# Kernel optimization log

Measured on AMD Instinct MI355X. Metric: run time of the kernel, lower is better.

Reference implementation:

```python
import jax, jax.numpy as jnp
import numpy as np

N_NODES = 50000
N_EDGES = 800000
D_IN = 128
D_HID = 128
D_OUT = 128
N_LAYERS = 2
NEG_SLOPE = 0.2


def leaky(x):
    return jnp.where(x >= 0, x, NEG_SLOPE * x)


def setup_inputs() -> dict:
    key = jax.random.key(0)
    ks = jax.random.split(key, 12)
    s = 1.0 / np.sqrt(D_HID)
    feats = jax.random.normal(ks[0], (N_NODES, D_IN), dtype=jnp.float32)
    src = jax.random.randint(ks[1], (N_EDGES,), 0, N_NODES)
    dst = jax.random.randint(ks[2], (N_EDGES,), 0, N_NODES)
    # SIRConv params per layer: W_Q (dst), W_K (src), W_R (output proj)
    Wq = jax.random.normal(ks[3], (N_LAYERS, D_IN, D_HID), dtype=jnp.float32) * s
    bq = jnp.zeros((N_LAYERS, D_HID), dtype=jnp.float32)
    Wk = jax.random.normal(ks[4], (N_LAYERS, D_IN, D_HID), dtype=jnp.float32) * s
    bk = jnp.zeros((N_LAYERS, D_HID), dtype=jnp.float32)
    Wr = jax.random.normal(ks[5], (N_LAYERS, D_HID, D_HID), dtype=jnp.float32) * s
    br = jnp.zeros((N_LAYERS, D_HID), dtype=jnp.float32)
    # Jumping-knowledge readouts: one per entry of feats_list (input + each layer);
    # input_dim == hidden_dim so weights stack along the leading axis.
    Wro = jax.random.normal(ks[6], (N_LAYERS + 1, D_HID, D_OUT), dtype=jnp.float32) * s
    bro = jnp.zeros((N_LAYERS + 1, D_OUT), dtype=jnp.float32)
    return {"feats": feats, "Wq": Wq, "bq": bq, "Wk": Wk, "bk": bk,
            "Wr": Wr, "br": br, "Wro": Wro, "bro": bro,
            "src": src, "dst": dst}


def reference(feats, Wq, bq, Wk, bk, Wr, br, Wro, bro, src, dst):
    # mean-aggregation denominator: in-degree, clamped to 1
    deg = jax.ops.segment_sum(jnp.ones((N_EDGES,), jnp.float32), dst,
                              num_segments=N_NODES)
    denom = jnp.maximum(deg, 1.0)[:, None]  # [N, 1]

    feats_list = [feats]
    h = feats
    for i in range(N_LAYERS):
        hq = h @ Wq[i] + bq[i]          # [N, H] (dst transform)
        hk = h @ Wk[i] + bk[i]          # [N, H] (src transform)
        m = leaky(hq[dst] + hk[src])    # [E, H] contextualized messages
        agg = jax.ops.segment_sum(m, dst, num_segments=N_NODES) / denom
        h = agg @ Wr[i] + br[i]         # conv output (+ residual = 0)
        h = leaky(h)                    # norm='none', dropout=0
        feats_list.append(h)

    # jumping-knowledge readout: sum of per-stage linear readouts
    score = feats_list[0] @ Wro[0] + bro[0]
    for i in range(1, N_LAYERS + 1):
        score = score + feats_list[i] @ Wro[i] + bro[i]
    return score
```

## Files before the change

### kernel.cpp

```cpp
#include <hip/hip_runtime.h>

#define NN 50000
#define NE 800000
#define D 128
#define NEG 0.2f

#define NEB 256
#define TILE1 3125
#define NB2 196
#define CAPB 128
#define NT64 782

#define SB_PREP 576
#define SB_CONV 6250
#define SB_TOTAL (SB_PREP + SB_CONV + NEB)

typedef short bf8_t __attribute__((ext_vector_type(8)));
typedef float f4_t __attribute__((ext_vector_type(4)));

__device__ __forceinline__ unsigned short f2bf(float f) {
  unsigned int u = __float_as_uint(f);
  return (unsigned short)((u + 0x7FFF + ((u >> 16) & 1)) >> 16);
}
__device__ __forceinline__ float bf2f(unsigned int b) { return __uint_as_float(b << 16); }

__device__ __forceinline__ f4_t MF(bf8_t a, bf8_t b, f4_t c) {
  return __builtin_amdgcn_mfma_f32_16x16x32_bf16(a, b, c, 0, 0, 0);
}

__device__ __forceinline__ int swz_u(int u) { return u ^ ((u >> 4) & 7); }

__device__ __forceinline__ int excl_scan256(int x, int t, int* wsum) {
  const int lane = t & 63, wave = t >> 6;
  int v = x;
#pragma unroll
  for (int off = 1; off < 64; off <<= 1) {
    int y = __shfl_up(v, off, 64);
    if (lane >= off) v += y;
  }
  if (lane == 63) wsum[wave] = v;
  __syncthreads();
  int wbase = 0;
  for (int w = 0; w < wave; ++w) wbase += wsum[w];
  return wbase + v - x;
}


__device__ __forceinline__ void stage_wh(unsigned short* wbuf,
                                         const unsigned short* __restrict__ WTh, int t) {
#pragma unroll
  for (int i = 0; i < 4; ++i) {
    int u = t + i * 256;
    *(uint4*)(wbuf + swz_u(u) * 8) = *(const uint4*)(WTh + u * 8);
  }
}

__device__ __forceinline__ void load_a16(const unsigned short* __restrict__ A,
                                         int base, int l15, int quad, bf8_t (&afr)[4]) {
  int r = base + l15;
  if (r >= NN) r = NN - 1;
  const unsigned short* p = A + (size_t)r * D + quad * 8;
#pragma unroll
  for (int kc = 0; kc < 4; ++kc) afr[kc] = *(const bf8_t*)(p + kc * 32);
}

__device__ __forceinline__ void load_a16_lds(const unsigned short* buf, int wave,
                                             int l15, int quad, bf8_t (&afr)[4]) {
  const int r = wave * 16 + l15;
#pragma unroll
  for (int kc = 0; kc < 4; ++kc)
    afr[kc] = *(const bf8_t*)(buf + swz_u(r * 16 + kc * 4 + quad) * 8);
}

__device__ __forceinline__ void tile16h(const unsigned short* wbuf, const bf8_t (&afr)[4],
                                        int l15, int quad, f4_t* acc4) {
#pragma unroll
  for (int kc = 0; kc < 4; ++kc)
#pragma unroll
    for (int nt = 0; nt < 4; ++nt) {
      bf8_t b = *(const bf8_t*)(wbuf + swz_u((nt * 16 + l15) * 16 + kc * 4 + quad) * 8);
      acc4[nt] = MF(afr[kc], b, acc4[nt]);
    }
}

__device__ __forceinline__ void store_c8(unsigned short* __restrict__ C,
                                         const float* __restrict__ bias,
                                         const f4_t (&acc)[8], int base, int l15,
                                         int quad, bool lk) {
#pragma unroll
  for (int j = 0; j < 8; ++j) {
    int col = (j >> 2) * 64 + (j & 3) * 16 + l15;
    float bb = bias[col];
#pragma unroll
    for (int reg = 0; reg < 4; ++reg) {
      int row = base + quad * 4 + reg;
      if (row < NN) {
        float v = acc[j][reg] + bb;
        if (lk) v = v >= 0.f ? v : NEG * v;
        C[(size_t)row * D + col] = f2bf(v);
      }
    }
  }
}

#define ACC_TO_ABUF(ACC, BIAS)                                        \
  {                                                                   \
    _Pragma("unroll") for (int j = 0; j < 8; ++j) {                   \
      int col = (j >> 2) * 64 + (j & 3) * 16 + l15;                   \
      float bb = (BIAS)[col];                                         \
      _Pragma("unroll") for (int reg = 0; reg < 4; ++reg) {           \
        int rl = wave * 16 + quad * 4 + reg;                          \
        float v = ACC[j][reg] + bb;                                   \
        v = v >= 0.f ? v : NEG * v;                                   \
        int s = rl * D + col;                                         \
        abuf[s ^ ((rl & 7) << 3)] = f2bf(v);                          \
      }                                                               \
    }                                                                 \
  }

__global__ __launch_bounds__(256) void setup(
    const float* __restrict__ Wq, const float* __restrict__ Wk,
    const float* __restrict__ Wr, const float* __restrict__ Wro,
    const float* __restrict__ feats, const int* __restrict__ src,
    const int* __restrict__ dst,
    unsigned short* __restrict__ WT, unsigned short* __restrict__ x0,
    unsigned int* __restrict__ ebuf2, int* __restrict__ H_T) {
  __shared__ int cnt[NB2];
  const int b = blockIdx.x;
  const int t = threadIdx.x;
  if (b < SB_PREP) {
    const int m = b >> 6, xb = b & 63;
    const float* sp;
    if (m < 2) sp = Wq + m * D * D;
    else if (m < 4) sp = Wk + (m - 2) * D * D;
    else if (m < 6) sp = Wr + (m - 4) * D * D;
    else sp = Wro + (m - 6) * D * D;
    const int n = xb * 2 + (t >> 7);
    const int k = t & 127;
    WT[(size_t)m * D * D + n * D + k] = f2bf(sp[k * D + n]);
  } else if (b < SB_PREP + SB_CONV) {
    int i = ((b - SB_PREP) * 256 + t) * 4;
    float4 v = *(const float4*)(feats + i);
    ushort4 o = {f2bf(v.x), f2bf(v.y), f2bf(v.z), f2bf(v.w)};
    *(ushort4*)(x0 + i) = o;
  } else {
    const int blk = b - SB_PREP - SB_CONV;
    if (t < NB2) cnt[t] = 0;
    __syncthreads();
    const int beg = blk * TILE1, end = beg + TILE1;
    for (int i = beg + t; i < end; i += 256) {
      unsigned int d = (unsigned int)dst[i];
      unsigned int s = (unsigned int)src[i];
      int bkt = (int)(d >> 8);
      int pos = atomicAdd(&cnt[bkt], 1);
      if (pos < CAPB)
        ebuf2[((size_t)bkt * NEB + blk) * CAPB + pos] = s | (d << 16);
    }
    __syncthreads();
    if (t < NB2) H_T[blk * NB2 + t] = cnt[t];
  }
}

__global__ __launch_bounds__(256) void sort_qk0(
    const int* __restrict__ H_T, const unsigned int* __restrict__ ebuf2,
    int* __restrict__ ssrc, int* __restrict__ rowptr, int* __restrict__ deg,
    const unsigned short* __restrict__ x0,
    const unsigned short* __restrict__ WTq, const float* __restrict__ bq_,
    const unsigned short* __restrict__ WTk, const float* __restrict__ bk_,
    unsigned short* __restrict__ hq, unsigned short* __restrict__ hk) {
  __shared__ __align__(16) unsigned char smraw[16384];
  const int t = threadIdx.x;
  const int gx = blockIdx.x;
  if (gx < NB2) {
    int* cnt = (int*)smraw;
    int* fill = cnt + 256;
    int* sc = fill + 256;
    int* wsum = sc + 256;
    const int b = gx;
    int tot = 0;
    if (t < NB2)
#pragma unroll 4
      for (int j = 0; j < NEB; ++j) tot += H_T[j * NB2 + t];
    int bbase = excl_scan256(tot, t, wsum);
    sc[t] = bbase;
    __syncthreads();
    const int beg = sc[b];
    int cj = H_T[t * NB2 + b];
    if (cj > CAPB) cj = CAPB;
    const unsigned int* cell = ebuf2 + ((size_t)b * NEB + t) * CAPB;
    cnt[t] = 0;
    __syncthreads();
    for (int i = 0; i < cj; ++i)
      atomicAdd(&cnt[(cell[i] >> 16) & 255], 1);
    __syncthreads();
    const int x = cnt[t];
    const int excl = excl_scan256(x, t, wsum);
    fill[t] = excl;
    const int node = (b << 8) + t;
    if (node < NN) {
      rowptr[node] = beg + excl;
      deg[node] = x;
    }
    if (b == 0 && t == 0) rowptr[NN] = NE;
    __syncthreads();
    for (int i = 0; i < cj; ++i) {
      unsigned int p = cell[i];
      int pos = atomicAdd(&fill[(p >> 16) & 255], 1);
      ssrc[beg + pos] = (int)(p & 0xFFFFu);
    }
  } else {
    unsigned short* wbuf = (unsigned short*)smraw;
    const int tile = gx - NB2;
    const int wave = t >> 6, lane = t & 63;
    const int l15 = lane & 15, quad = lane >> 4;
    const int base = tile * 64 + wave * 16;
    bf8_t afr[4];
    load_a16(x0, base, l15, quad, afr);
    stage_wh(wbuf, WTq, t);
    __syncthreads();
    f4_t aq[8] = {};
    tile16h(wbuf, afr, l15, quad, aq);
    __syncthreads();
    stage_wh(wbuf, WTq + 64 * D, t);
    __syncthreads();
    tile16h(wbuf, afr, l15, quad, aq + 4);
    store_c8(hq, bq_, aq, base, l15, quad, false);
    __syncthreads();
    stage_wh(wbuf, WTk, t);
    __syncthreads();
    f4_t ak[8] = {};
    tile16h(wbuf, afr, l15, quad, ak);
    __syncthreads();
    stage_wh(wbuf, WTk + 64 * D, t);
    __syncthreads();
    tile16h(wbuf, afr, l15, quad, ak + 4);
    store_c8(hk, bk_, ak, base, l15, quad, false);
  }
}

#define PROC(kb)                                                     \
  {                                                                  \
    float m;                                                         \
    m = q[0] + bf2f(kb.x & 0xFFFFu); a[0] += m >= 0.f ? m : NEG * m; \
    m = q[1] + bf2f(kb.x >> 16);     a[1] += m >= 0.f ? m : NEG * m; \
    m = q[2] + bf2f(kb.y & 0xFFFFu); a[2] += m >= 0.f ? m : NEG * m; \
    m = q[3] + bf2f(kb.y >> 16);     a[3] += m >= 0.f ? m : NEG * m; \
    m = q[4] + bf2f(kb.z & 0xFFFFu); a[4] += m >= 0.f ? m : NEG * m; \
    m = q[5] + bf2f(kb.z >> 16);     a[5] += m >= 0.f ? m : NEG * m; \
    m = q[6] + bf2f(kb.w & 0xFFFFu); a[6] += m >= 0.f ? m : NEG * m; \
    m = q[7] + bf2f(kb.w >> 16);     a[7] += m >= 0.f ? m : NEG * m; \
  }

__global__ __launch_bounds__(256) void aggregate(
    const int* __restrict__ rowptr, const int* __restrict__ ssrc,
    const int* __restrict__ deg,
    const unsigned short* __restrict__ hq, const unsigned short* __restrict__ hk,
    unsigned short* __restrict__ ag) {
  const int wave = threadIdx.x >> 6, lane = threadIdx.x & 63;
  const int v = blockIdx.x * 4 + wave;
  if (v >= NN) return;
  const int sub = lane & 15, grp = lane >> 4;
  const int beg = rowptr[v], end = rowptr[v + 1];

  uint4 qb = *(const uint4*)(hq + (size_t)v * D + sub * 8);
  float q[8];
  q[0] = bf2f(qb.x & 0xFFFFu); q[1] = bf2f(qb.x >> 16);
  q[2] = bf2f(qb.y & 0xFFFFu); q[3] = bf2f(qb.y >> 16);
  q[4] = bf2f(qb.z & 0xFFFFu); q[5] = bf2f(qb.z >> 16);
  q[6] = bf2f(qb.w & 0xFFFFu); q[7] = bf2f(qb.w >> 16);

  float a[8] = {0.f, 0.f, 0.f, 0.f, 0.f, 0.f, 0.f, 0.f};
  int e = beg + grp;
  for (; e + 12 < end; e += 16) {
    int s0 = ssrc[e];
    int s1 = ssrc[e + 4];
    int s2 = ssrc[e + 8];
    int s3 = ssrc[e + 12];
    uint4 k0 = *(const uint4*)(hk + (size_t)s0 * D + sub * 8);
    uint4 k1 = *(const uint4*)(hk + (size_t)s1 * D + sub * 8);
    uint4 k2 = *(const uint4*)(hk + (size_t)s2 * D + sub * 8);
    uint4 k3 = *(const uint4*)(hk + (size_t)s3 * D + sub * 8);
    PROC(k0);
    PROC(k1);
    PROC(k2);
    PROC(k3);
  }
  for (; e + 4 < end; e += 8) {
    int s0 = ssrc[e];
    int s1 = ssrc[e + 4];
    uint4 k0 = *(const uint4*)(hk + (size_t)s0 * D + sub * 8);
    uint4 k1 = *(const uint4*)(hk + (size_t)s1 * D + sub * 8);
    PROC(k0);
    PROC(k1);
  }
  if (e < end) {
    int s0 = ssrc[e];
    uint4 k0 = *(const uint4*)(hk + (size_t)s0 * D + sub * 8);
    PROC(k0);
  }
#pragma unroll
  for (int j = 0; j < 8; ++j) {
    a[j] += __shfl_xor(a[j], 16, 64);
    a[j] += __shfl_xor(a[j], 32, 64);
  }
  if (grp == 0) {
    float inv = 1.f / fmaxf((float)deg[v], 1.f);
    uint4 o;
    o.x = (unsigned int)f2bf(a[0] * inv) | ((unsigned int)f2bf(a[1] * inv) << 16);
    o.y = (unsigned int)f2bf(a[2] * inv) | ((unsigned int)f2bf(a[3] * inv) << 16);
    o.z = (unsigned int)f2bf(a[4] * inv) | ((unsigned int)f2bf(a[5] * inv) << 16);
    o.w = (unsigned int)f2bf(a[6] * inv) | ((unsigned int)f2bf(a[7] * inv) << 16);
    *(uint4*)(ag + (size_t)v * D + sub * 8) = o;
  }
}

__global__ __launch_bounds__(256) void wr_qk1(
    const unsigned short* __restrict__ ag,
    const unsigned short* __restrict__ WTr, const float* __restrict__ brr,
    unsigned short* __restrict__ h1,
    const unsigned short* __restrict__ WTq, const float* __restrict__ bq1,
    unsigned short* __restrict__ hq,
    const unsigned short* __restrict__ WTk, const float* __restrict__ bk1,
    unsigned short* __restrict__ hk) {
  __shared__ unsigned short wbuf[64 * D];
  __shared__ unsigned short abuf[64 * D];
  const int t = threadIdx.x, wave = t >> 6, lane = t & 63;
  const int l15 = lane & 15, quad = lane >> 4;
  const int tb = blockIdx.x * 64;
  const int base = tb + wave * 16;

  bf8_t afr[4];
  load_a16(ag, base, l15, quad, afr);
  stage_wh(wbuf, WTr, t);
  __syncthreads();
  f4_t acc[8] = {};
  tile16h(wbuf, afr, l15, quad, acc);
  __syncthreads();
  stage_wh(wbuf, WTr + 64 * D, t);
  __syncthreads();
  tile16h(wbuf, afr, l15, quad, acc + 4);

  ACC_TO_ABUF(acc, brr);
  __syncthreads();

  bf8_t hfr[4];
  load_a16_lds(abuf, wave, l15, quad, hfr);
#pragma unroll
  for (int i = 0; i < 4; ++i) {
    int u = t + i * 256;
    int row = tb + (u >> 4);
    if (row < NN)
      *(uint4*)(h1 + (size_t)tb * D + u * 8) = *(const uint4*)(abuf + swz_u(u) * 8);
  }

  stage_wh(wbuf, WTq, t);
  __syncthreads();
  f4_t aq[8] = {};
  tile16h(wbuf, hfr, l15, quad, aq);
  __syncthreads();
  stage_wh(wbuf, WTq + 64 * D, t);
  __syncthreads();
  tile16h(wbuf, hfr, l15, quad, aq + 4);
  store_c8(hq, bq1, aq, base, l15, quad, false);
  __syncthreads();

  stage_wh(wbuf, WTk, t);
  __syncthreads();
  f4_t ak[8] = {};
  tile16h(wbuf, hfr, l15, quad, ak);
  __syncthreads();
  stage_wh(wbuf, WTk + 64 * D, t);
  __syncthreads();
  tile16h(wbuf, hfr, l15, quad, ak + 4);
  store_c8(hk, bk1, ak, base, l15, quad, false);
}

__global__ __launch_bounds__(256) void wr_ro(
    const unsigned short* __restrict__ ag,
    const unsigned short* __restrict__ WTr, const float* __restrict__ brr,
    const unsigned short* __restrict__ x0,
    const unsigned short* __restrict__ h1,
    const unsigned short* __restrict__ WTro, const float* __restrict__ bro_,
    float* __restrict__ out) {
  __shared__ unsigned short wbuf[64 * D];
  __shared__ unsigned short abuf[64 * D];
  const int t = threadIdx.x, wave = t >> 6, lane = t & 63;
  const int l15 = lane & 15, quad = lane >> 4;
  const int tb = blockIdx.x * 64;
  const int base = tb + wave * 16;
  const size_t WM = (size_t)D * D;

  bf8_t afr[4];
  load_a16(ag, base, l15, quad, afr);
  stage_wh(wbuf, WTr, t);
  __syncthreads();
  f4_t acch[8] = {};
  tile16h(wbuf, afr, l15, quad, acch);
  __syncthreads();
  stage_wh(wbuf, WTr + 64 * D, t);
  __syncthreads();
  tile16h(wbuf, afr, l15, quad, acch + 4);

  ACC_TO_ABUF(acch, brr);
  __syncthreads();

  bf8_t hfr[4];
  load_a16_lds(abuf, wave, l15, quad, hfr);
  f4_t acc[8] = {};

  stage_wh(wbuf, WTro + 2 * WM, t);
  __syncthreads();
  tile16h(wbuf, hfr, l15, quad, acc);
  __syncthreads();
  stage_wh(wbuf, WTro + 2 * WM + 64 * D, t);
  __syncthreads();
  tile16h(wbuf, hfr, l15, quad, acc + 4);
  __syncthreads();

  load_a16(x0, base, l15, quad, afr);
  stage_wh(wbuf, WTro, t);
  __syncthreads();
  tile16h(wbuf, afr, l15, quad, acc);
  __syncthreads();
  stage_wh(wbuf, WTro + 64 * D, t);
  __syncthreads();
  tile16h(wbuf, afr, l15, quad, acc + 4);
  __syncthreads();

  load_a16(h1, base, l15, quad, afr);
  stage_wh(wbuf, WTro + WM, t);
  __syncthreads();
  tile16h(wbuf, afr, l15, quad, acc);
  __syncthreads();
  stage_wh(wbuf, WTro + WM + 64 * D, t);
  __syncthreads();
  tile16h(wbuf, afr, l15, quad, acc + 4);

#pragma unroll
  for (int j = 0; j < 8; ++j) {
    int col = (j >> 2) * 64 + (j & 3) * 16 + l15;
    float bsum = bro_[col] + bro_[D + col] + bro_[2 * D + col];
#pragma unroll
    for (int reg = 0; reg < 4; ++reg) {
      int row = base + quad * 4 + reg;
      if (row < NN) out[(size_t)row * D + col] = acc[j][reg] + bsum;
    }
  }
}

extern "C" void kernel_launch(void* const* d_in, const int* in_sizes, int n_in,
                              void* d_out, int out_size, void* d_ws, size_t ws_size,
                              hipStream_t stream) {
  const float* feats = (const float*)d_in[0];
  const float* Wq = (const float*)d_in[1];
  const float* bq = (const float*)d_in[2];
  const float* Wk = (const float*)d_in[3];
  const float* bk = (const float*)d_in[4];
  const float* Wr = (const float*)d_in[5];
  const float* br = (const float*)d_in[6];
  const float* Wro = (const float*)d_in[7];
  const float* bro = (const float*)d_in[8];
  const int* src = (const int*)d_in[9];
  const int* dst = (const int*)d_in[10];
  float* out = (float*)d_out;

  size_t off = 0;
  char* base = (char*)d_ws;
  auto alloc = [&](size_t bytes) -> void* {
    void* p = base + off;
    off += (bytes + 255) & ~(size_t)255;
    return p;
  };
  int* H_T = (int*)alloc((size_t)NEB * NB2 * 4);
  unsigned int* ebuf2 = (unsigned int*)alloc((size_t)NB2 * NEB * CAPB * 4);
  int* ssrc = (int*)alloc((size_t)NE * 4);
  int* rowptr = (int*)alloc((size_t)(NN + 1) * 4);
  int* deg = (int*)alloc((size_t)NN * 4);
  unsigned short* WT = (unsigned short*)alloc((size_t)9 * D * D * 2);
  unsigned short* x0 = (unsigned short*)alloc((size_t)NN * D * 2);
  unsigned short* hq = (unsigned short*)alloc((size_t)NN * D * 2);
  unsigned short* hk = (unsigned short*)alloc((size_t)NN * D * 2);
  unsigned short* ag = (unsigned short*)alloc((size_t)NN * D * 2);
  unsigned short* h1 = (unsigned short*)alloc((size_t)NN * D * 2);

  const size_t WM = (size_t)D * D;
  const int ab = (NN + 3) / 4;

  setup<<<SB_TOTAL, 256, 0, stream>>>(Wq, Wk, Wr, Wro, feats, src, dst,
                                      WT, x0, ebuf2, H_T);
  sort_qk0<<<NB2 + NT64, 256, 0, stream>>>(H_T, ebuf2, ssrc, rowptr, deg,
                                           x0, WT + 0 * WM, bq, WT + 2 * WM, bk,
                                           hq, hk);
  aggregate<<<ab, 256, 0, stream>>>(rowptr, ssrc, deg, hq, hk, ag);
  wr_qk1<<<NT64, 256, 0, stream>>>(ag, WT + 4 * WM, br, h1,
                                   WT + 1 * WM, bq + D, hq,
                                   WT + 3 * WM, bk + D, hk);
  aggregate<<<ab, 256, 0, stream>>>(rowptr, ssrc, deg, hq, hk, ag);
  wr_ro<<<NT64, 256, 0, stream>>>(ag, WT + 5 * WM, br + D, x0, h1,
                                  WT + 6 * WM, bro, out);
}
```

Before: 263.2 us.

## Finer edge binning with atomic bucket totals and split Q/K projection blocks

Edge binning now uses 1024 smaller edge tiles with a smaller per-cell capacity, and these blocks are scheduled first in the setup grid. Each tile adds its per-bucket counts into a global total with atomics, so the sort kernel no longer sums a column of the count table per bucket. Each sort block now walks four cells per thread. The layer-0 Q and K projections are split into separate blocks, doubling the GEMM grid and halving per-block serial work. The cost is an extra memset launch, global atomics, and more per-bucket cells to scan in the sort.

Measured after the change: 267.2 us. Within noise of the previous version (+1.5%).

```diff
diff --git a/kernel.cpp b/kernel.cpp
--- a/kernel.cpp
+++ b/kernel.cpp
@@ -5,15 +5,15 @@
 #define D 128
 #define NEG 0.2f
 
-#define NEB 256
-#define TILE1 3125
+#define NEB 1024
+#define TILE1 782
 #define NB2 196
-#define CAPB 128
+#define CAPB 32
 #define NT64 782
 
 #define SB_PREP 576
 #define SB_CONV 6250
-#define SB_TOTAL (SB_PREP + SB_CONV + NEB)
+#define SB_TOTAL (NEB + SB_PREP + SB_CONV)
 
 typedef short bf8_t __attribute__((ext_vector_type(8)));
 typedef float f4_t __attribute__((ext_vector_type(4)));
@@ -124,12 +124,34 @@
     const float* __restrict__ feats, const int* __restrict__ src,
     const int* __restrict__ dst,
     unsigned short* __restrict__ WT, unsigned short* __restrict__ x0,
-    unsigned int* __restrict__ ebuf2, int* __restrict__ H_T) {
+    unsigned int* __restrict__ ebuf2, int* __restrict__ H_T,
+    int* __restrict__ btot) {
   __shared__ int cnt[NB2];
   const int b = blockIdx.x;
   const int t = threadIdx.x;
-  if (b < SB_PREP) {
-    const int m = b >> 6, xb = b & 63;
+  if (b < NEB) {
+    const int blk = b;
+    if (t < NB2) cnt[t] = 0;
+    __syncthreads();
+    const int beg = blk * TILE1;
+    int end = beg + TILE1;
+    if (end > NE) end = NE;
+    for (int i = beg + t; i < end; i += 256) {
+      unsigned int d = (unsigned int)dst[i];
+      unsigned int s = (unsigned int)src[i];
+      int bkt = (int)(d >> 8);
+      int pos = atomicAdd(&cnt[bkt], 1);
+      if (pos < CAPB)
+        ebuf2[((size_t)bkt * NEB + blk) * CAPB + pos] = s | (d << 16);
+    }
+    __syncthreads();
+    if (t < NB2) {
+      H_T[blk * NB2 + t] = cnt[t];
+      if (cnt[t]) atomicAdd(&btot[t], cnt[t]);
+    }
+  } else if (b < NEB + SB_PREP) {
+    const int pb = b - NEB;
+    const int m = pb >> 6, xb = pb & 63;
     const float* sp;
     if (m < 2) sp = Wq + m * D * D;
     else if (m < 4) sp = Wk + (m - 2) * D * D;
@@ -138,31 +160,17 @@
     const int n = xb * 2 + (t >> 7);
     const int k = t & 127;
     WT[(size_t)m * D * D + n * D + k] = f2bf(sp[k * D + n]);
-  } else if (b < SB_PREP + SB_CONV) {
-    int i = ((b - SB_PREP) * 256 + t) * 4;
+  } else {
+    int i = ((b - NEB - SB_PREP) * 256 + t) * 4;
     float4 v = *(const float4*)(feats + i);
     ushort4 o = {f2bf(v.x), f2bf(v.y), f2bf(v.z), f2bf(v.w)};
     *(ushort4*)(x0 + i) = o;
-  } else {
-    const int blk = b - SB_PREP - SB_CONV;
-    if (t < NB2) cnt[t] = 0;
-    __syncthreads();
-    const int beg = blk * TILE1, end = beg + TILE1;
-    for (int i = beg + t; i < end; i += 256) {
-      unsigned int d = (unsigned int)dst[i];
-      unsigned int s = (unsigned int)src[i];
-      int bkt = (int)(d >> 8);
-      int pos = atomicAdd(&cnt[bkt], 1);
-      if (pos < CAPB)
-        ebuf2[((size_t)bkt * NEB + blk) * CAPB + pos] = s | (d << 16);
-    }
-    __syncthreads();
-    if (t < NB2) H_T[blk * NB2 + t] = cnt[t];
   }
 }
 
 __global__ __launch_bounds__(256) void sort_qk0(
-    const int* __restrict__ H_T, const unsigned int* __restrict__ ebuf2,
+    const int* __restrict__ H_T, const int* __restrict__ btot,
+    const unsigned int* __restrict__ ebuf2,
     int* __restrict__ ssrc, int* __restrict__ rowptr, int* __restrict__ deg,
     const unsigned short* __restrict__ x0,
     const unsigned short* __restrict__ WTq, const float* __restrict__ bq_,
@@ -177,21 +185,26 @@
     int* sc = fill + 256;
     int* wsum = sc + 256;
     const int b = gx;
-    int tot = 0;
-    if (t < NB2)
-#pragma unroll 4
-      for (int j = 0; j < NEB; ++j) tot += H_T[j * NB2 + t];
+    int tot = (t < NB2) ? btot[t] : 0;
     int bbase = excl_scan256(tot, t, wsum);
     sc[t] = bbase;
     __syncthreads();
     const int beg = sc[b];
-    int cj = H_T[t * NB2 + b];
-    if (cj > CAPB) cj = CAPB;
-    const unsigned int* cell = ebuf2 + ((size_t)b * NEB + t) * CAPB;
+    int cj[4];
+    const unsigned int* cell[4];
+#pragma unroll
+    for (int c = 0; c < 4; ++c) {
+      int blk = t + 256 * c;
+      int n = H_T[blk * NB2 + b];
+      cj[c] = n > CAPB ? CAPB : n;
+      cell[c] = ebuf2 + ((size_t)b * NEB + blk) * CAPB;
+    }
     cnt[t] = 0;
     __syncthreads();
-    for (int i = 0; i < cj; ++i)
-      atomicAdd(&cnt[(cell[i] >> 16) & 255], 1);
+#pragma unroll
+    for (int c = 0; c < 4; ++c)
+      for (int i = 0; i < cj[c]; ++i)
+        atomicAdd(&cnt[(cell[c][i] >> 16) & 255], 1);
     __syncthreads();
     const int x = cnt[t];
     const int excl = excl_scan256(x, t, wsum);
@@ -203,38 +216,32 @@
     }
     if (b == 0 && t == 0) rowptr[NN] = NE;
     __syncthreads();
-    for (int i = 0; i < cj; ++i) {
-      unsigned int p = cell[i];
-      int pos = atomicAdd(&fill[(p >> 16) & 255], 1);
-      ssrc[beg + pos] = (int)(p & 0xFFFFu);
-    }
+#pragma unroll
+    for (int c = 0; c < 4; ++c)
+      for (int i = 0; i < cj[c]; ++i) {
+        unsigned int p = cell[c][i];
+        int pos = atomicAdd(&fill[(p >> 16) & 255], 1);
+        ssrc[beg + pos] = (int)(p & 0xFFFFu);
+      }
   } else {
     unsigned short* wbuf = (unsigned short*)smraw;
-    const int tile = gx - NB2;
+    const int g = gx - NB2;
+    const int sel = g & 1, tile = g >> 1;
     const int wave = t >> 6, lane = t & 63;
     const int l15 = lane & 15, quad = lane >> 4;
     const int base = tile * 64 + wave * 16;
+    const unsigned short* WT_ = sel ? WTk : WTq;
     bf8_t afr[4];
     load_a16(x0, base, l15, quad, afr);
-    stage_wh(wbuf, WTq, t);
-    __syncthreads();
-    f4_t aq[8] = {};
-    tile16h(wbuf, afr, l15, quad, aq);
-    __syncthreads();
-    stage_wh(wbuf, WTq + 64 * D, t);
-    __syncthreads();
-    tile16h(wbuf, afr, l15, quad, aq + 4);
-    store_c8(hq, bq_, aq, base, l15, quad, false);
-    __syncthreads();
-    stage_wh(wbuf, WTk, t);
-    __syncthreads();
-    f4_t ak[8] = {};
-    tile16h(wbuf, afr, l15, quad, ak);
-    __syncthreads();
-    stage_wh(wbuf, WTk + 64 * D, t);
-    __syncthreads();
-    tile16h(wbuf, afr, l15, quad, ak + 4);
-    store_c8(hk, bk_, ak, base, l15, quad, false);
+    stage_wh(wbuf, WT_, t);
+    __syncthreads();
+    f4_t acc[8] = {};
+    tile16h(wbuf, afr, l15, quad, acc);
+    __syncthreads();
+    stage_wh(wbuf, WT_ + 64 * D, t);
+    __syncthreads();
+    tile16h(wbuf, afr, l15, quad, acc + 4);
+    store_c8(sel ? hk : hq, sel ? bk_ : bq_, acc, base, l15, quad, false);
   }
 }
 
@@ -472,6 +479,7 @@
     return p;
   };
   int* H_T = (int*)alloc((size_t)NEB * NB2 * 4);
+  int* btot = (int*)alloc((size_t)NB2 * 4);
   unsigned int* ebuf2 = (unsigned int*)alloc((size_t)NB2 * NEB * CAPB * 4);
   int* ssrc = (int*)alloc((size_t)NE * 4);
   int* rowptr = (int*)alloc((size_t)(NN + 1) * 4);
@@ -486,11 +494,12 @@
   const size_t WM = (size_t)D * D;
   const int ab = (NN + 3) / 4;
 
+  hipMemsetAsync(btot, 0, (size_t)NB2 * 4, stream);
   setup<<<SB_TOTAL, 256, 0, stream>>>(Wq, Wk, Wr, Wro, feats, src, dst,
-                                      WT, x0, ebuf2, H_T);
-  sort_qk0<<<NB2 + NT64, 256, 0, stream>>>(H_T, ebuf2, ssrc, rowptr, deg,
-                                           x0, WT + 0 * WM, bq, WT + 2 * WM, bk,
-                                           hq, hk);
+                                      WT, x0, ebuf2, H_T, btot);
+  sort_qk0<<<NB2 + 2 * NT64, 256, 0, stream>>>(H_T, btot, ebuf2, ssrc, rowptr, deg,
+                                               x0, WT + 0 * WM, bq, WT + 2 * WM, bk,
+                                               hq, hk);
   aggregate<<<ab, 256, 0, stream>>>(rowptr, ssrc, deg, hq, hk, ag);
   wr_qk1<<<NT64, 256, 0, stream>>>(ag, WT + 4 * WM, br, h1,
                                    WT + 1 * WM, bq + D, hq,
```
